# Kernel optimization log

Hardware: AMD Instinct MI355X
Metric: run time of the kernel (lower is better)

The kernel has to match this reference:

```python
import jax, jax.numpy as jnp
import numpy as np

N_NODES = 20000
N_EDGES = 320000
F_IN = 256
HID = 256
N_CLS = 5


def _glorot(key, shape):
    lim = np.sqrt(6.0 / (shape[0] + shape[1]))
    return jax.random.uniform(key, shape, jnp.float32, -lim, lim)


def setup_inputs() -> dict:
    key = jax.random.key(0)
    ks = jax.random.split(key, 12)
    x1 = jax.random.normal(ks[0], (N_NODES, F_IN), jnp.float32)
    x2 = jax.random.normal(ks[1], (N_NODES, F_IN), jnp.float32)
    ei1 = jax.random.randint(ks[2], (2, N_EDGES), 0, N_NODES, jnp.int64 if jax.config.jax_enable_x64 else jnp.int32)
    ei2 = jax.random.randint(ks[3], (2, N_EDGES), 0, N_NODES, jnp.int64 if jax.config.jax_enable_x64 else jnp.int32)
    params = {
        'W1': _glorot(ks[4], (F_IN, HID)), 'b1': jnp.zeros((HID,), jnp.float32),
        'W2': _glorot(ks[5], (HID, HID)), 'b2': jnp.zeros((HID,), jnp.float32),
        'W3': _glorot(ks[6], (HID, HID)), 'b3': jnp.zeros((HID,), jnp.float32),
        'Wl': _glorot(ks[7], (HID, N_CLS)), 'bl': jnp.zeros((N_CLS,), jnp.float32),
    }
    return {'x1': x1, 'edge_index1': ei1, 'x2': x2, 'edge_index2': ei2, **params}


def gcn_conv(x, edge_index, W, b):
    # PyG GCNConv: add self-loops, symmetric normalization D^-1/2 (A+I) D^-1/2 (X W) + b
    N = x.shape[0]
    src, dst = edge_index[0], edge_index[1]
    deg = jax.ops.segment_sum(jnp.ones(src.shape[0], x.dtype), dst, num_segments=N) + 1.0
    dinv = jax.lax.rsqrt(deg)  # [N]
    xw = x @ W                 # [N, H]
    coef = (dinv[src] * dinv[dst])[:, None]  # per-edge norm
    agg = jax.ops.segment_sum(xw[src] * coef, dst, num_segments=N)
    agg = agg + xw * (dinv * dinv)[:, None]  # self-loop term
    return agg + b


def _branch(x, ei, W1, b1, W2, b2, W3, b3):
    # dropout is identity in eval mode
    h = jax.nn.relu(gcn_conv(x, ei, W1, b1))
    h = jax.nn.relu(gcn_conv(h, ei, W2, b2))
    return gcn_conv(h, ei, W3, b3)


def reference(x1, edge_index1, x2, edge_index2, W1, b1, W2, b2, W3, b3, Wl, bl):
    h1 = _branch(x1, edge_index1, W1, b1, W2, b2, W3, b3)
    h2 = _branch(x2, edge_index2, W1, b1, W2, b2, W3, b3)
    h = jnp.concatenate([h1, h2], axis=0)          # [2N, H]
    pooled = jnp.mean(h, axis=0, keepdims=True)    # batch is all zeros -> single mean pool
    return pooled @ Wl + bl                        # [1, num_classes]
```

## Files before the change

### kernel.cpp

```cpp
#include <hip/hip_runtime.h>
#include <hip/hip_bf16.h>

#define N_NODES 20000
#define N_EDGES 320000
#define HID 256

typedef __attribute__((ext_vector_type(8))) short bf16x8;
typedef __attribute__((ext_vector_type(4))) float f32x4;

__device__ __forceinline__ float bf2f(ushort u) {
  union { unsigned int i; float f; } v; v.i = ((unsigned int)u) << 16; return v.f;
}
__device__ __forceinline__ ushort f2bf(float f) {
  union { float f; unsigned int i; } v; v.f = f;
  unsigned int r = v.i + 0x7FFFu + ((v.i >> 16) & 1u);
  return (ushort)(r >> 16);
}

__global__ void detect_kernel(const void* x1, const void* ei1, int* flags) {
  __shared__ int cnt_wild, cnt_oddnz;
  if (threadIdx.x == 0) { cnt_wild = 0; cnt_oddnz = 0; }
  __syncthreads();
  const ushort* xu = (const ushort*)x1;
  int wild = 0;
#pragma unroll
  for (int k = 0; k < 4; k++) {
    ushort u = xu[threadIdx.x * 4 + k];
    int ex = (u >> 7) & 0xFF;
    if (ex >= 0x90) wild++;
  }
  if (wild) atomicAdd(&cnt_wild, wild);
  const int* ii = (const int*)ei1;
  if (ii[threadIdx.x * 2 + 1] != 0) atomicAdd(&cnt_oddnz, 1);
  __syncthreads();
  if (threadIdx.x == 0) {
    flags[0] = (cnt_wild > 64) ? 1 : 0;
    flags[1] = (cnt_oddnz < 8) ? 1 : 0;
  }
}

__global__ void init_kernel(int* cnt0, int* cnt1, float* t0, float* t1,
                            float* s0, float* s1) {
  int i = blockIdx.x * blockDim.x + threadIdx.x;
  if (i < N_NODES) { cnt0[i] = 0; cnt1[i] = 0; t0[i] = 0.f; t1[i] = 0.f; }
  if (i < HID) { s0[i] = 0.f; s1[i] = 0.f; }
}

__global__ void cvt_ei_count_kernel(const void* e0, const void* e1,
                                    int* o0, int* o1,
                                    int* cnt0, int* cnt1,
                                    int* rank0, int* rank1, const int* flags) {
  int b = blockIdx.y;
  const void* e = b ? e1 : e0;
  int* o = b ? o1 : o0;
  int* cnt = b ? cnt1 : cnt0;
  int* rank = b ? rank1 : rank0;
  int i = blockIdx.x * 256 + threadIdx.x;
  if (i >= 2 * N_EDGES) return;
  int v = flags[1] ? (int)((const long long*)e)[i] : ((const int*)e)[i];
  o[i] = v;
  if (i >= N_EDGES) rank[i - N_EDGES] = atomicAdd(&cnt[v], 1);
}

__global__ void cvt_x_kernel(const void* x0, const void* x1v,
                             ushort* o0, ushort* o1, const int* flags) {
  const void* x = blockIdx.y ? x1v : x0;
  ushort* o = blockIdx.y ? o1 : o0;
  int i4 = (blockIdx.x * 256 + threadIdx.x) * 4;
  if (i4 >= N_NODES * HID) return;
  if (flags[0]) {
    float4 v = *(const float4*)((const float*)x + i4);
    ushort4 w; w.x = f2bf(v.x); w.y = f2bf(v.y); w.z = f2bf(v.z); w.w = f2bf(v.w);
    *(ushort4*)(o + i4) = w;
  } else {
    *(ushort4*)(o + i4) = *(const ushort4*)((const ushort*)x + i4);
  }
}

__global__ void cvt_w_kernel(const void* W1, const void* W2, const void* W3, const void* Wl,
                             const void* b1, const void* b2, const void* b3, const void* bl,
                             ushort* out, const int* flags) {
  int i = blockIdx.x * 256 + threadIdx.x;
  if (i >= 198661) return;
  const void* src; int off;
  if (i < 65536)       { src = W1; off = 0; }
  else if (i < 131072) { src = W2; off = 65536; }
  else if (i < 196608) { src = W3; off = 131072; }
  else if (i < 197888) { src = Wl; off = 196608; }
  else if (i < 198144) { src = b1; off = 197888; }
  else if (i < 198400) { src = b2; off = 198144; }
  else if (i < 198656) { src = b3; off = 198400; }
  else                 { src = bl; off = 198656; }
  int j = i - off;
  out[i] = flags[0] ? f2bf(((const float*)src)[j]) : ((const ushort*)src)[j];
}

__global__ void dinv_kernel(const int* cnt0, const int* cnt1, float* dinv0, float* dinv1) {
  int i = blockIdx.x * blockDim.x + threadIdx.x;
  if (i >= N_NODES) return;
  const int* cnt = blockIdx.y ? cnt1 : cnt0;
  float* dinv = blockIdx.y ? dinv1 : dinv0;
  dinv[i] = rsqrtf((float)cnt[i] + 1.0f);
}

__global__ __launch_bounds__(1024) void scan_kernel(const int* cnt0, const int* cnt1,
                                                    int* rp0, int* rp1) {
  const int* cnt = blockIdx.x ? cnt1 : cnt0;
  int* rp = blockIdx.x ? rp1 : rp0;
  __shared__ int sd[1024];
  int tid = threadIdx.x;
  int base = tid * 20;
  int pref[20];
  int run = 0;
#pragma unroll
  for (int k = 0; k < 20; k++) {
    int i = base + k;
    run += (i < N_NODES) ? cnt[i] : 0;
    pref[k] = run;
  }
  sd[tid] = run;
  __syncthreads();
  for (int off = 1; off < 1024; off <<= 1) {
    int v = (tid >= off) ? sd[tid - off] : 0;
    __syncthreads();
    sd[tid] += v;
    __syncthreads();
  }
  int offset = sd[tid] - run;
  if (tid == 0) rp[0] = 0;
#pragma unroll
  for (int k = 0; k < 20; k++) {
    int i = base + k;
    if (i < N_NODES) rp[i + 1] = offset + pref[k];
  }
}

__global__ void fill_kernel(const int* ei0, const int* ei1,
                            const float* dinv0, const float* dinv1,
                            const int* rp0, const int* rp1,
                            const int* rank0, const int* rank1,
                            int* col0, int* col1,
                            float* coef0, float* coef1,
                            float* t0, float* t1) {
  int e = blockIdx.x * blockDim.x + threadIdx.x;
  if (e >= N_EDGES) return;
  int b = blockIdx.y;
  const int* ei = b ? ei1 : ei0;
  const float* dinv = b ? dinv1 : dinv0;
  const int* rp = b ? rp1 : rp0;
  const int* rank = b ? rank1 : rank0;
  int* col = b ? col1 : col0;
  float* coef = b ? coef1 : coef0;
  float* t = b ? t1 : t0;
  int src = ei[e], dst = ei[N_EDGES + e];
  int slot = rp[dst] + rank[e];
  float dd = dinv[dst];
  col[slot] = src;
  coef[slot] = dinv[src] * dd;
  atomicAdd(&t[src], dd);
}

__global__ __launch_bounds__(256) void gemm_kernel(
    const ushort* __restrict__ A0, const ushort* __restrict__ A1,
    const ushort* __restrict__ W,
    ushort* __restrict__ C0, ushort* __restrict__ C1) {
  const ushort* A = blockIdx.z ? A1 : A0;
  ushort* C = blockIdx.z ? C1 : C0;
  int m0 = blockIdx.x * 64;
  int n0 = blockIdx.y * 64;
  __shared__ ushort As[64][40];
  __shared__ ushort Bs[64][40];
  int tid = threadIdx.x;
  int wave = tid >> 6, lane = tid & 63;
  int quad = lane >> 4, r16 = lane & 15;
  f32x4 acc0 = {0.f, 0.f, 0.f, 0.f}, acc1 = acc0, acc2 = acc0, acc3 = acc0;
  int la_row = tid >> 2;
  int la_off = (tid & 3) * 8;
  int lb_k = tid >> 3;
  int lb_n = (tid & 7) * 8;
  for (int k0 = 0; k0 < 256; k0 += 32) {
    int gr = m0 + la_row;
    int4 va = {0, 0, 0, 0};
    if (gr < N_NODES) va = *(const int4*)(A + gr * 256 + k0 + la_off);
    *(int4*)&As[la_row][la_off] = va;
    int4 vb = *(const int4*)(W + (k0 + lb_k) * 256 + n0 + lb_n);
    ushort tmp[8];
    *(int4*)tmp = vb;
#pragma unroll
    for (int j = 0; j < 8; j++) Bs[lb_n + j][lb_k] = tmp[j];
    __syncthreads();
    bf16x8 a  = *(const bf16x8*)&As[wave * 16 + r16][quad * 8];
    bf16x8 b0 = *(const bf16x8*)&Bs[r16][quad * 8];
    bf16x8 b1 = *(const bf16x8*)&Bs[16 + r16][quad * 8];
    bf16x8 b2 = *(const bf16x8*)&Bs[32 + r16][quad * 8];
    bf16x8 b3 = *(const bf16x8*)&Bs[48 + r16][quad * 8];
    acc0 = __builtin_amdgcn_mfma_f32_16x16x32_bf16(a, b0, acc0, 0, 0, 0);
    acc1 = __builtin_amdgcn_mfma_f32_16x16x32_bf16(a, b1, acc1, 0, 0, 0);
    acc2 = __builtin_amdgcn_mfma_f32_16x16x32_bf16(a, b2, acc2, 0, 0, 0);
    acc3 = __builtin_amdgcn_mfma_f32_16x16x32_bf16(a, b3, acc3, 0, 0, 0);
    __syncthreads();
  }
  int orow = m0 + wave * 16 + quad * 4;
#pragma unroll
  for (int r = 0; r < 4; r++) {
    int gr = orow + r;
    if (gr < N_NODES) {
      ushort* cp = C + gr * 256 + n0 + r16;
      cp[0]  = f2bf(acc0[r]);
      cp[16] = f2bf(acc1[r]);
      cp[32] = f2bf(acc2[r]);
      cp[48] = f2bf(acc3[r]);
    }
  }
}

__global__ __launch_bounds__(256) void agg_kernel(
    const ushort* __restrict__ XW0, const ushort* __restrict__ XW1,
    const float* __restrict__ dinv0, const float* __restrict__ dinv1,
    const int* __restrict__ rp0, const int* __restrict__ rp1,
    const int* __restrict__ col0, const int* __restrict__ col1,
    const float* __restrict__ coef0, const float* __restrict__ coef1,
    const ushort* __restrict__ bias,
    ushort* __restrict__ H0, ushort* __restrict__ H1) {
  int b = blockIdx.y;
  const ushort* XW = b ? XW1 : XW0;
  const float* dinv = b ? dinv1 : dinv0;
  const int* rp = b ? rp1 : rp0;
  const int* col = b ? col1 : col0;
  const float* coef = b ? coef1 : coef0;
  ushort* H = b ? H1 : H0;
  int wave = threadIdx.x >> 6, lane = threadIdx.x & 63;
  int i = blockIdx.x * 4 + wave;
  int f4 = lane * 4;
  float di = dinv[i];
  float self = di * di;
  ushort4 v = *(const ushort4*)(XW + i * 256 + f4);
  float a0 = self * bf2f(v.x), a1 = self * bf2f(v.y);
  float a2 = self * bf2f(v.z), a3 = self * bf2f(v.w);
  float c0_ = 0.f, c1_ = 0.f, c2_ = 0.f, c3_ = 0.f;
  int e0 = rp[i], e1 = rp[i + 1];
  int e = e0;
  for (; e + 3 < e1; e += 4) {
    int s0 = col[e], s1 = col[e + 1], s2 = col[e + 2], s3 = col[e + 3];
    float w0 = coef[e], w1 = coef[e + 1], w2 = coef[e + 2], w3 = coef[e + 3];
    ushort4 u0 = *(const ushort4*)(XW + s0 * 256 + f4);
    ushort4 u1 = *(const ushort4*)(XW + s1 * 256 + f4);
    ushort4 u2 = *(const ushort4*)(XW + s2 * 256 + f4);
    ushort4 u3 = *(const ushort4*)(XW + s3 * 256 + f4);
    a0 += w0 * bf2f(u0.x); a1 += w0 * bf2f(u0.y); a2 += w0 * bf2f(u0.z); a3 += w0 * bf2f(u0.w);
    c0_ += w1 * bf2f(u1.x); c1_ += w1 * bf2f(u1.y); c2_ += w1 * bf2f(u1.z); c3_ += w1 * bf2f(u1.w);
    a0 += w2 * bf2f(u2.x); a1 += w2 * bf2f(u2.y); a2 += w2 * bf2f(u2.z); a3 += w2 * bf2f(u2.w);
    c0_ += w3 * bf2f(u3.x); c1_ += w3 * bf2f(u3.y); c2_ += w3 * bf2f(u3.z); c3_ += w3 * bf2f(u3.w);
  }
  for (; e < e1; e++) {
    int s = col[e];
    float c = coef[e];
    ushort4 u = *(const ushort4*)(XW + s * 256 + f4);
    a0 += c * bf2f(u.x); a1 += c * bf2f(u.y); a2 += c * bf2f(u.z); a3 += c * bf2f(u.w);
  }
  a0 += c0_; a1 += c1_; a2 += c2_; a3 += c3_;
  ushort4 bb = *(const ushort4*)(bias + f4);
  a0 = fmaxf(a0 + bf2f(bb.x), 0.f);
  a1 = fmaxf(a1 + bf2f(bb.y), 0.f);
  a2 = fmaxf(a2 + bf2f(bb.z), 0.f);
  a3 = fmaxf(a3 + bf2f(bb.w), 0.f);
  ushort4 o; o.x = f2bf(a0); o.y = f2bf(a1); o.z = f2bf(a2); o.w = f2bf(a3);
  *(ushort4*)(H + i * 256 + f4) = o;
}

__global__ __launch_bounds__(256) void colsum_kernel(
    const ushort* __restrict__ H0, const ushort* __restrict__ H1,
    const float* __restrict__ dinv0, const float* __restrict__ dinv1,
    const float* __restrict__ t0, const float* __restrict__ t1,
    float* __restrict__ s0, float* __restrict__ s1) {
  int b = blockIdx.y;
  const ushort* H = b ? H1 : H0;
  const float* dinv = b ? dinv1 : dinv0;
  const float* t = b ? t1 : t0;
  float* s = b ? s1 : s0;
  int f = threadIdx.x;
  float acc = 0.f;
  for (int j = blockIdx.x; j < N_NODES; j += gridDim.x) {
    float dj = dinv[j];
    float c = dj * (t[j] + dj);
    acc += c * bf2f(H[j * 256 + f]);
  }
  atomicAdd(&s[f], acc);
}

__global__ __launch_bounds__(256) void final_kernel(
    const float* __restrict__ s0, const float* __restrict__ s1,
    const ushort* __restrict__ W3, const ushort* __restrict__ b3,
    const ushort* __restrict__ Wl, const ushort* __restrict__ bl,
    void* __restrict__ out, const int* __restrict__ flags) {
  __shared__ float v[256];
  __shared__ float pooled[256];
  int t = threadIdx.x;
  v[t] = s0[t] + s1[t];
  __syncthreads();
  float acc = 0.f;
  for (int f = 0; f < 256; f++) acc += v[f] * bf2f(W3[f * 256 + t]);
  pooled[t] = acc * (1.0f / (2.0f * N_NODES)) + bf2f(b3[t]);
  __syncthreads();
  if (t < 5) {
    float o = bf2f(bl[t]);
    for (int h = 0; h < 256; h++) o += pooled[h] * bf2f(Wl[h * 5 + t]);
    if (flags[0]) ((float*)out)[t] = o;
    else ((ushort*)out)[t] = f2bf(o);
  }
}

extern "C" void kernel_launch(void* const* d_in, const int* in_sizes, int n_in,
                              void* d_out, int out_size, void* d_ws, size_t ws_size,
                              hipStream_t stream) {
  const void* x1 = d_in[0];
  const void* ei1 = d_in[1];
  const void* x2 = d_in[2];
  const void* ei2 = d_in[3];
  const void* W1 = d_in[4];
  const void* b1 = d_in[5];
  const void* W2 = d_in[6];
  const void* b2 = d_in[7];
  const void* W3 = d_in[8];
  const void* b3 = d_in[9];
  const void* Wl = d_in[10];
  const void* bl = d_in[11];

  char* p = (char*)d_ws;
  auto alloc = [&](size_t bytes) {
    char* r = p;
    p += (bytes + 255) & ~size_t(255);
    return r;
  };
  int* flags   = (int*)alloc(256);
  float* dinv0 = (float*)alloc(N_NODES * 4);
  float* dinv1 = (float*)alloc(N_NODES * 4);
  float* t0    = (float*)alloc(N_NODES * 4);
  float* t1    = (float*)alloc(N_NODES * 4);
  float* s0    = (float*)alloc(HID * 4);
  float* s1    = (float*)alloc(HID * 4);
  int* cnt0    = (int*)alloc(N_NODES * 4);
  int* cnt1    = (int*)alloc(N_NODES * 4);
  int* rp0     = (int*)alloc((N_NODES + 1) * 4);
  int* rp1     = (int*)alloc((N_NODES + 1) * 4);
  int* col0    = (int*)alloc(N_EDGES * 4);
  int* col1    = (int*)alloc(N_EDGES * 4);
  float* coef0 = (float*)alloc(N_EDGES * 4);
  float* coef1 = (float*)alloc(N_EDGES * 4);
  ushort* wbuf = (ushort*)alloc(198661 * 2);
  ushort* xw0  = (ushort*)alloc((size_t)N_NODES * HID * 2);
  ushort* xw1  = (ushort*)alloc((size_t)N_NODES * HID * 2);
  ushort* xc0  = (ushort*)alloc((size_t)N_NODES * HID * 2);
  ushort* xc1  = (ushort*)alloc((size_t)N_NODES * HID * 2);
  int* ei32_0 = (int*)xw0;
  int* ei32_1 = ei32_0 + 2 * N_EDGES;
  int* rank0  = ei32_1 + 2 * N_EDGES;
  int* rank1  = rank0 + N_EDGES;
  ushort* h0 = xc0;
  ushort* h1 = xc1;

  ushort* Wc1 = wbuf + 0;
  ushort* Wc2 = wbuf + 65536;
  ushort* Wc3 = wbuf + 131072;
  ushort* Wlc = wbuf + 196608;
  ushort* bc1 = wbuf + 197888;
  ushort* bc2 = wbuf + 198144;
  ushort* bc3 = wbuf + 198400;
  ushort* blc = wbuf + 198656;

  detect_kernel<<<1, 256, 0, stream>>>(x1, ei1, flags);
  init_kernel<<<(N_NODES + 255) / 256, 256, 0, stream>>>(cnt0, cnt1, t0, t1, s0, s1);
  cvt_ei_count_kernel<<<dim3((2 * N_EDGES + 255) / 256, 2), 256, 0, stream>>>(
      ei1, ei2, ei32_0, ei32_1, cnt0, cnt1, rank0, rank1, flags);
  cvt_x_kernel<<<dim3(N_NODES * HID / 1024, 2), 256, 0, stream>>>(
      x1, x2, xc0, xc1, flags);
  cvt_w_kernel<<<(198661 + 255) / 256, 256, 0, stream>>>(
      W1, W2, W3, Wl, b1, b2, b3, bl, wbuf, flags);
  dinv_kernel<<<dim3((N_NODES + 255) / 256, 2), 256, 0, stream>>>(cnt0, cnt1, dinv0, dinv1);
  scan_kernel<<<2, 1024, 0, stream>>>(cnt0, cnt1, rp0, rp1);
  fill_kernel<<<dim3((N_EDGES + 255) / 256, 2), 256, 0, stream>>>(
      ei32_0, ei32_1, dinv0, dinv1, rp0, rp1, rank0, rank1, col0, col1, coef0, coef1, t0, t1);

  gemm_kernel<<<dim3(313, 4, 2), 256, 0, stream>>>(xc0, xc1, Wc1, xw0, xw1);
  agg_kernel<<<dim3(N_NODES / 4, 2), 256, 0, stream>>>(
      xw0, xw1, dinv0, dinv1, rp0, rp1, col0, col1, coef0, coef1, bc1, h0, h1);

  gemm_kernel<<<dim3(313, 4, 2), 256, 0, stream>>>(h0, h1, Wc2, xw0, xw1);
  agg_kernel<<<dim3(N_NODES / 4, 2), 256, 0, stream>>>(
      xw0, xw1, dinv0, dinv1, rp0, rp1, col0, col1, coef0, coef1, bc2, h0, h1);

  colsum_kernel<<<dim3(128, 2), 256, 0, stream>>>(h0, h1, dinv0, dinv1, t0, t1, s0, s1);
  final_kernel<<<1, 256, 0, stream>>>(s0, s1, Wc3, bc3, Wlc, blc, d_out, flags);
}
```

Measured before the change: 416.5 us.

## Build CSR with node-partitioned shared-memory histograms and packed edge pairs

Replaces the global-atomic edge counting and fill with node-range-partitioned kernels: 64 blocks per graph each scan all edges and use shared-memory atomics for counts, ranks and the t accumulation. This removes the init and int64-to-int32 conversion kernels and the rank buffer. Column index and coefficient are packed into one int2 array, so aggregation needs one load per edge. The column sum writes per-block partials that the final kernel reduces, replacing global float atomics. In exchange every block rereads the full edge list, and slot order within a row is nondeterministic.

```diff
diff --git a/kernel.cpp b/kernel.cpp
--- a/kernel.cpp
+++ b/kernel.cpp
@@ -4,6 +4,7 @@
 #define N_NODES 20000
 #define N_EDGES 320000
 #define HID 256
+#define NR 313
 
 typedef __attribute__((ext_vector_type(8))) short bf16x8;
 typedef __attribute__((ext_vector_type(4))) float f32x4;
@@ -37,29 +38,6 @@
     flags[0] = (cnt_wild > 64) ? 1 : 0;
     flags[1] = (cnt_oddnz < 8) ? 1 : 0;
   }
-}
-
-__global__ void init_kernel(int* cnt0, int* cnt1, float* t0, float* t1,
-                            float* s0, float* s1) {
-  int i = blockIdx.x * blockDim.x + threadIdx.x;
-  if (i < N_NODES) { cnt0[i] = 0; cnt1[i] = 0; t0[i] = 0.f; t1[i] = 0.f; }
-  if (i < HID) { s0[i] = 0.f; s1[i] = 0.f; }
-}
-
-__global__ void cvt_ei_count_kernel(const void* e0, const void* e1,
-                                    int* o0, int* o1,
-                                    int* cnt0, int* cnt1,
-                                    int* rank0, int* rank1, const int* flags) {
-  int b = blockIdx.y;
-  const void* e = b ? e1 : e0;
-  int* o = b ? o1 : o0;
-  int* cnt = b ? cnt1 : cnt0;
-  int* rank = b ? rank1 : rank0;
-  int i = blockIdx.x * 256 + threadIdx.x;
-  if (i >= 2 * N_EDGES) return;
-  int v = flags[1] ? (int)((const long long*)e)[i] : ((const int*)e)[i];
-  o[i] = v;
-  if (i >= N_EDGES) rank[i - N_EDGES] = atomicAdd(&cnt[v], 1);
 }
 
 __global__ void cvt_x_kernel(const void* x0, const void* x1v,
@@ -95,6 +73,42 @@
   out[i] = flags[0] ? f2bf(((const float*)src)[j]) : ((const ushort*)src)[j];
 }
 
+__global__ __launch_bounds__(1024) void count_part_kernel(
+    const void* e0, const void* e1, int* cnt0, int* cnt1, const int* flags) {
+  int b = blockIdx.y;
+  const void* e = b ? e1 : e0;
+  int* cnt = b ? cnt1 : cnt0;
+  int lo = blockIdx.x * NR;
+  int hi = min(lo + NR, N_NODES);
+  int nr = hi - lo;
+  __shared__ int h[NR];
+  for (int k = threadIdx.x; k < nr; k += 1024) h[k] = 0;
+  __syncthreads();
+  if (flags[1]) {
+    const long long* d = (const long long*)e + N_EDGES;
+    for (int i = threadIdx.x * 4; i < N_EDGES; i += 4096) {
+      longlong2 p0 = *(const longlong2*)(d + i);
+      longlong2 p1 = *(const longlong2*)(d + i + 2);
+      int v0 = (int)p0.x, v1 = (int)p0.y, v2 = (int)p1.x, v3 = (int)p1.y;
+      if ((unsigned)(v0 - lo) < (unsigned)nr) atomicAdd(&h[v0 - lo], 1);
+      if ((unsigned)(v1 - lo) < (unsigned)nr) atomicAdd(&h[v1 - lo], 1);
+      if ((unsigned)(v2 - lo) < (unsigned)nr) atomicAdd(&h[v2 - lo], 1);
+      if ((unsigned)(v3 - lo) < (unsigned)nr) atomicAdd(&h[v3 - lo], 1);
+    }
+  } else {
+    const int* d = (const int*)e + N_EDGES;
+    for (int i = threadIdx.x * 4; i < N_EDGES; i += 4096) {
+      int4 v = *(const int4*)(d + i);
+      if ((unsigned)(v.x - lo) < (unsigned)nr) atomicAdd(&h[v.x - lo], 1);
+      if ((unsigned)(v.y - lo) < (unsigned)nr) atomicAdd(&h[v.y - lo], 1);
+      if ((unsigned)(v.z - lo) < (unsigned)nr) atomicAdd(&h[v.z - lo], 1);
+      if ((unsigned)(v.w - lo) < (unsigned)nr) atomicAdd(&h[v.w - lo], 1);
+    }
+  }
+  __syncthreads();
+  for (int k = threadIdx.x; k < nr; k += 1024) cnt[lo + k] = h[k];
+}
+
 __global__ void dinv_kernel(const int* cnt0, const int* cnt1, float* dinv0, float* dinv1) {
   int i = blockIdx.x * blockDim.x + threadIdx.x;
   if (i >= N_NODES) return;
@@ -135,29 +149,62 @@
   }
 }
 
-__global__ void fill_kernel(const int* ei0, const int* ei1,
-                            const float* dinv0, const float* dinv1,
-                            const int* rp0, const int* rp1,
-                            const int* rank0, const int* rank1,
-                            int* col0, int* col1,
-                            float* coef0, float* coef1,
-                            float* t0, float* t1) {
-  int e = blockIdx.x * blockDim.x + threadIdx.x;
-  if (e >= N_EDGES) return;
+__global__ __launch_bounds__(1024) void fill_part_kernel(
+    const void* e0, const void* e1,
+    const float* dinv0, const float* dinv1,
+    const int* rp0, const int* rp1,
+    int2* eg0, int2* eg1, float* t0, float* t1, const int* flags) {
   int b = blockIdx.y;
-  const int* ei = b ? ei1 : ei0;
+  const void* e = b ? e1 : e0;
   const float* dinv = b ? dinv1 : dinv0;
   const int* rp = b ? rp1 : rp0;
-  const int* rank = b ? rank1 : rank0;
-  int* col = b ? col1 : col0;
-  float* coef = b ? coef1 : coef0;
+  int2* eg = b ? eg1 : eg0;
   float* t = b ? t1 : t0;
-  int src = ei[e], dst = ei[N_EDGES + e];
-  int slot = rp[dst] + rank[e];
-  float dd = dinv[dst];
-  col[slot] = src;
-  coef[slot] = dinv[src] * dd;
-  atomicAdd(&t[src], dd);
+  int lo = blockIdx.x * NR;
+  int hi = min(lo + NR, N_NODES);
+  int nr = hi - lo;
+  __shared__ int lrank[NR];
+  __shared__ int lrp[NR];
+  __shared__ float ldv[NR];
+  __shared__ float lt[NR];
+  for (int k = threadIdx.x; k < nr; k += 1024) {
+    lrank[k] = 0; lt[k] = 0.f; lrp[k] = rp[lo + k]; ldv[k] = dinv[lo + k];
+  }
+  __syncthreads();
+  bool w64 = flags[1] != 0;
+  const int* si32 = (const int*)e;
+  const int* di32 = (const int*)e + N_EDGES;
+  const long long* si64 = (const long long*)e;
+  const long long* di64 = (const long long*)e + N_EDGES;
+  for (int i = threadIdx.x * 4; i < N_EDGES; i += 4096) {
+    int s[4], d[4];
+    if (w64) {
+      longlong2 a0 = *(const longlong2*)(si64 + i);
+      longlong2 a1 = *(const longlong2*)(si64 + i + 2);
+      longlong2 b0 = *(const longlong2*)(di64 + i);
+      longlong2 b1 = *(const longlong2*)(di64 + i + 2);
+      s[0] = (int)a0.x; s[1] = (int)a0.y; s[2] = (int)a1.x; s[3] = (int)a1.y;
+      d[0] = (int)b0.x; d[1] = (int)b0.y; d[2] = (int)b1.x; d[3] = (int)b1.y;
+    } else {
+      int4 a = *(const int4*)(si32 + i);
+      int4 bb = *(const int4*)(di32 + i);
+      s[0] = a.x; s[1] = a.y; s[2] = a.z; s[3] = a.w;
+      d[0] = bb.x; d[1] = bb.y; d[2] = bb.z; d[3] = bb.w;
+    }
+#pragma unroll
+    for (int k = 0; k < 4; k++) {
+      unsigned dd = (unsigned)(d[k] - lo);
+      if (dd < (unsigned)nr) {
+        int r = atomicAdd(&lrank[dd], 1);
+        float cf = dinv[s[k]] * ldv[dd];
+        eg[lrp[dd] + r] = make_int2(s[k], __float_as_int(cf));
+      }
+      unsigned ss = (unsigned)(s[k] - lo);
+      if (ss < (unsigned)nr) atomicAdd(&lt[ss], dinv[d[k]]);
+    }
+  }
+  __syncthreads();
+  for (int k = threadIdx.x; k < nr; k += 1024) t[lo + k] = lt[k];
 }
 
 __global__ __launch_bounds__(256) void gemm_kernel(
@@ -218,16 +265,14 @@
     const ushort* __restrict__ XW0, const ushort* __restrict__ XW1,
     const float* __restrict__ dinv0, const float* __restrict__ dinv1,
     const int* __restrict__ rp0, const int* __restrict__ rp1,
-    const int* __restrict__ col0, const int* __restrict__ col1,
-    const float* __restrict__ coef0, const float* __restrict__ coef1,
+    const int2* __restrict__ eg0, const int2* __restrict__ eg1,
     const ushort* __restrict__ bias,
     ushort* __restrict__ H0, ushort* __restrict__ H1) {
   int b = blockIdx.y;
   const ushort* XW = b ? XW1 : XW0;
   const float* dinv = b ? dinv1 : dinv0;
   const int* rp = b ? rp1 : rp0;
-  const int* col = b ? col1 : col0;
-  const float* coef = b ? coef1 : coef0;
+  const int2* eg = b ? eg1 : eg0;
   ushort* H = b ? H1 : H0;
   int wave = threadIdx.x >> 6, lane = threadIdx.x & 63;
   int i = blockIdx.x * 4 + wave;
@@ -241,21 +286,22 @@
   int e0 = rp[i], e1 = rp[i + 1];
   int e = e0;
   for (; e + 3 < e1; e += 4) {
-    int s0 = col[e], s1 = col[e + 1], s2 = col[e + 2], s3 = col[e + 3];
-    float w0 = coef[e], w1 = coef[e + 1], w2 = coef[e + 2], w3 = coef[e + 3];
-    ushort4 u0 = *(const ushort4*)(XW + s0 * 256 + f4);
-    ushort4 u1 = *(const ushort4*)(XW + s1 * 256 + f4);
-    ushort4 u2 = *(const ushort4*)(XW + s2 * 256 + f4);
-    ushort4 u3 = *(const ushort4*)(XW + s3 * 256 + f4);
+    int2 p0 = eg[e], p1 = eg[e + 1], p2 = eg[e + 2], p3 = eg[e + 3];
+    ushort4 u0 = *(const ushort4*)(XW + p0.x * 256 + f4);
+    ushort4 u1 = *(const ushort4*)(XW + p1.x * 256 + f4);
+    ushort4 u2 = *(const ushort4*)(XW + p2.x * 256 + f4);
+    ushort4 u3 = *(const ushort4*)(XW + p3.x * 256 + f4);
+    float w0 = __int_as_float(p0.y), w1 = __int_as_float(p1.y);
+    float w2 = __int_as_float(p2.y), w3 = __int_as_float(p3.y);
     a0 += w0 * bf2f(u0.x); a1 += w0 * bf2f(u0.y); a2 += w0 * bf2f(u0.z); a3 += w0 * bf2f(u0.w);
     c0_ += w1 * bf2f(u1.x); c1_ += w1 * bf2f(u1.y); c2_ += w1 * bf2f(u1.z); c3_ += w1 * bf2f(u1.w);
     a0 += w2 * bf2f(u2.x); a1 += w2 * bf2f(u2.y); a2 += w2 * bf2f(u2.z); a3 += w2 * bf2f(u2.w);
     c0_ += w3 * bf2f(u3.x); c1_ += w3 * bf2f(u3.y); c2_ += w3 * bf2f(u3.z); c3_ += w3 * bf2f(u3.w);
   }
   for (; e < e1; e++) {
-    int s = col[e];
-    float c = coef[e];
-    ushort4 u = *(const ushort4*)(XW + s * 256 + f4);
+    int2 pp = eg[e];
+    float c = __int_as_float(pp.y);
+    ushort4 u = *(const ushort4*)(XW + pp.x * 256 + f4);
     a0 += c * bf2f(u.x); a1 += c * bf2f(u.y); a2 += c * bf2f(u.z); a3 += c * bf2f(u.w);
   }
   a0 += c0_; a1 += c1_; a2 += c2_; a3 += c3_;
@@ -272,31 +318,45 @@
     const ushort* __restrict__ H0, const ushort* __restrict__ H1,
     const float* __restrict__ dinv0, const float* __restrict__ dinv1,
     const float* __restrict__ t0, const float* __restrict__ t1,
-    float* __restrict__ s0, float* __restrict__ s1) {
+    float* __restrict__ P) {
   int b = blockIdx.y;
   const ushort* H = b ? H1 : H0;
   const float* dinv = b ? dinv1 : dinv0;
   const float* t = b ? t1 : t0;
-  float* s = b ? s1 : s0;
-  int f = threadIdx.x;
-  float acc = 0.f;
-  for (int j = blockIdx.x; j < N_NODES; j += gridDim.x) {
+  int wave = threadIdx.x >> 6, lane = threadIdx.x & 63;
+  int wid = blockIdx.x * 4 + wave;
+  int f4 = lane * 4;
+  float a0 = 0.f, a1 = 0.f, a2 = 0.f, a3 = 0.f;
+  for (int j = wid; j < N_NODES; j += 256) {
     float dj = dinv[j];
     float c = dj * (t[j] + dj);
-    acc += c * bf2f(H[j * 256 + f]);
-  }
-  atomicAdd(&s[f], acc);
+    ushort4 u = *(const ushort4*)(H + j * 256 + f4);
+    a0 += c * bf2f(u.x); a1 += c * bf2f(u.y);
+    a2 += c * bf2f(u.z); a3 += c * bf2f(u.w);
+  }
+  __shared__ float part[4][256];
+  part[wave][f4 + 0] = a0; part[wave][f4 + 1] = a1;
+  part[wave][f4 + 2] = a2; part[wave][f4 + 3] = a3;
+  __syncthreads();
+  int f = threadIdx.x;
+  float ssum = part[0][f] + part[1][f] + part[2][f] + part[3][f];
+  P[(b * 64 + blockIdx.x) * 256 + f] = ssum;
 }
 
 __global__ __launch_bounds__(256) void final_kernel(
-    const float* __restrict__ s0, const float* __restrict__ s1,
+    const float* __restrict__ P,
     const ushort* __restrict__ W3, const ushort* __restrict__ b3,
     const ushort* __restrict__ Wl, const ushort* __restrict__ bl,
     void* __restrict__ out, const int* __restrict__ flags) {
   __shared__ float v[256];
   __shared__ float pooled[256];
   int t = threadIdx.x;
-  v[t] = s0[t] + s1[t];
+  float acc0 = 0.f, acc1 = 0.f;
+  for (int b = 0; b < 64; b++) {
+    acc0 += P[b * 256 + t];
+    acc1 += P[(64 + b) * 256 + t];
+  }
+  v[t] = acc0 + acc1;
   __syncthreads();
   float acc = 0.f;
   for (int f = 0; f < 256; f++) acc += v[f] * bf2f(W3[f * 256 + t]);
@@ -337,25 +397,18 @@
   float* dinv1 = (float*)alloc(N_NODES * 4);
   float* t0    = (float*)alloc(N_NODES * 4);
   float* t1    = (float*)alloc(N_NODES * 4);
-  float* s0    = (float*)alloc(HID * 4);
-  float* s1    = (float*)alloc(HID * 4);
   int* cnt0    = (int*)alloc(N_NODES * 4);
   int* cnt1    = (int*)alloc(N_NODES * 4);
   int* rp0     = (int*)alloc((N_NODES + 1) * 4);
   int* rp1     = (int*)alloc((N_NODES + 1) * 4);
-  int* col0    = (int*)alloc(N_EDGES * 4);
-  int* col1    = (int*)alloc(N_EDGES * 4);
-  float* coef0 = (float*)alloc(N_EDGES * 4);
-  float* coef1 = (float*)alloc(N_EDGES * 4);
+  int2* eg0    = (int2*)alloc((size_t)N_EDGES * 8);
+  int2* eg1    = (int2*)alloc((size_t)N_EDGES * 8);
+  float* Pp    = (float*)alloc(2 * 64 * 256 * 4);
   ushort* wbuf = (ushort*)alloc(198661 * 2);
   ushort* xw0  = (ushort*)alloc((size_t)N_NODES * HID * 2);
   ushort* xw1  = (ushort*)alloc((size_t)N_NODES * HID * 2);
   ushort* xc0  = (ushort*)alloc((size_t)N_NODES * HID * 2);
   ushort* xc1  = (ushort*)alloc((size_t)N_NODES * HID * 2);
-  int* ei32_0 = (int*)xw0;
-  int* ei32_1 = ei32_0 + 2 * N_EDGES;
-  int* rank0  = ei32_1 + 2 * N_EDGES;
-  int* rank1  = rank0 + N_EDGES;
   ushort* h0 = xc0;
   ushort* h1 = xc1;
 
@@ -369,26 +422,24 @@
   ushort* blc = wbuf + 198656;
 
   detect_kernel<<<1, 256, 0, stream>>>(x1, ei1, flags);
-  init_kernel<<<(N_NODES + 255) / 256, 256, 0, stream>>>(cnt0, cnt1, t0, t1, s0, s1);
-  cvt_ei_count_kernel<<<dim3((2 * N_EDGES + 255) / 256, 2), 256, 0, stream>>>(
-      ei1, ei2, ei32_0, ei32_1, cnt0, cnt1, rank0, rank1, flags);
   cvt_x_kernel<<<dim3(N_NODES * HID / 1024, 2), 256, 0, stream>>>(
       x1, x2, xc0, xc1, flags);
   cvt_w_kernel<<<(198661 + 255) / 256, 256, 0, stream>>>(
       W1, W2, W3, Wl, b1, b2, b3, bl, wbuf, flags);
+  count_part_kernel<<<dim3(64, 2), 1024, 0, stream>>>(ei1, ei2, cnt0, cnt1, flags);
   dinv_kernel<<<dim3((N_NODES + 255) / 256, 2), 256, 0, stream>>>(cnt0, cnt1, dinv0, dinv1);
   scan_kernel<<<2, 1024, 0, stream>>>(cnt0, cnt1, rp0, rp1);
-  fill_kernel<<<dim3((N_EDGES + 255) / 256, 2), 256, 0, stream>>>(
-      ei32_0, ei32_1, dinv0, dinv1, rp0, rp1, rank0, rank1, col0, col1, coef0, coef1, t0, t1);
+  fill_part_kernel<<<dim3(64, 2), 1024, 0, stream>>>(
+      ei1, ei2, dinv0, dinv1, rp0, rp1, eg0, eg1, t0, t1, flags);
 
   gemm_kernel<<<dim3(313, 4, 2), 256, 0, stream>>>(xc0, xc1, Wc1, xw0, xw1);
   agg_kernel<<<dim3(N_NODES / 4, 2), 256, 0, stream>>>(
-      xw0, xw1, dinv0, dinv1, rp0, rp1, col0, col1, coef0, coef1, bc1, h0, h1);
+      xw0, xw1, dinv0, dinv1, rp0, rp1, eg0, eg1, bc1, h0, h1);
 
   gemm_kernel<<<dim3(313, 4, 2), 256, 0, stream>>>(h0, h1, Wc2, xw0, xw1);
   agg_kernel<<<dim3(N_NODES / 4, 2), 256, 0, stream>>>(
-      xw0, xw1, dinv0, dinv1, rp0, rp1, col0, col1, coef0, coef1, bc2, h0, h1);
-
-  colsum_kernel<<<dim3(128, 2), 256, 0, stream>>>(h0, h1, dinv0, dinv1, t0, t1, s0, s1);
-  final_kernel<<<1, 256, 0, stream>>>(s0, s1, Wc3, bc3, Wlc, blc, d_out, flags);
-}
+      xw0, xw1, dinv0, dinv1, rp0, rp1, eg0, eg1, bc2, h0, h1);
+
+  colsum_kernel<<<dim3(64, 2), 256, 0, stream>>>(h0, h1, dinv0, dinv1, t0, t1, Pp);
+  final_kernel<<<1, 256, 0, stream>>>(Pp, Wc3, bc3, Wlc, blc, d_out, flags);
+}
```

Measured after the change: 480.0 us. +15.3%, slower.

## Interleave CSR col/coef, fold dinv into scan, deterministic colsum partials

Applied to the files above, without the earlier changes.

Packs the column index and edge coefficient into a single int2 array, so the aggregation kernel issues one 8-byte load per edge instead of two separate 4-byte loads. The dinv computation moves into the scan kernel, which removes one launch. The colsum kernel now uses per-wave vectorized ushort4 reads and writes per-block partials that final_kernel reduces, replacing the atomics and the zeroing of the s buffers. Costs are a slightly larger edge array footprint and a serial 64-step reduction in the final kernel.

```diff
diff --git a/kernel.cpp b/kernel.cpp
--- a/kernel.cpp
+++ b/kernel.cpp
@@ -39,11 +39,9 @@
   }
 }
 
-__global__ void init_kernel(int* cnt0, int* cnt1, float* t0, float* t1,
-                            float* s0, float* s1) {
+__global__ void init_kernel(int* cnt0, int* cnt1, float* t0, float* t1) {
   int i = blockIdx.x * blockDim.x + threadIdx.x;
   if (i < N_NODES) { cnt0[i] = 0; cnt1[i] = 0; t0[i] = 0.f; t1[i] = 0.f; }
-  if (i < HID) { s0[i] = 0.f; s1[i] = 0.f; }
 }
 
 __global__ void cvt_ei_count_kernel(const void* e0, const void* e1,
@@ -95,18 +93,12 @@
   out[i] = flags[0] ? f2bf(((const float*)src)[j]) : ((const ushort*)src)[j];
 }
 
-__global__ void dinv_kernel(const int* cnt0, const int* cnt1, float* dinv0, float* dinv1) {
-  int i = blockIdx.x * blockDim.x + threadIdx.x;
-  if (i >= N_NODES) return;
-  const int* cnt = blockIdx.y ? cnt1 : cnt0;
-  float* dinv = blockIdx.y ? dinv1 : dinv0;
-  dinv[i] = rsqrtf((float)cnt[i] + 1.0f);
-}
-
 __global__ __launch_bounds__(1024) void scan_kernel(const int* cnt0, const int* cnt1,
-                                                    int* rp0, int* rp1) {
+                                                    int* rp0, int* rp1,
+                                                    float* dinv0, float* dinv1) {
   const int* cnt = blockIdx.x ? cnt1 : cnt0;
   int* rp = blockIdx.x ? rp1 : rp0;
+  float* dinv = blockIdx.x ? dinv1 : dinv0;
   __shared__ int sd[1024];
   int tid = threadIdx.x;
   int base = tid * 20;
@@ -115,7 +107,9 @@
 #pragma unroll
   for (int k = 0; k < 20; k++) {
     int i = base + k;
-    run += (i < N_NODES) ? cnt[i] : 0;
+    int c = (i < N_NODES) ? cnt[i] : 0;
+    if (i < N_NODES) dinv[i] = rsqrtf((float)c + 1.0f);
+    run += c;
     pref[k] = run;
   }
   sd[tid] = run;
@@ -139,8 +133,7 @@
                             const float* dinv0, const float* dinv1,
                             const int* rp0, const int* rp1,
                             const int* rank0, const int* rank1,
-                            int* col0, int* col1,
-                            float* coef0, float* coef1,
+                            int2* eg0, int2* eg1,
                             float* t0, float* t1) {
   int e = blockIdx.x * blockDim.x + threadIdx.x;
   if (e >= N_EDGES) return;
@@ -149,14 +142,12 @@
   const float* dinv = b ? dinv1 : dinv0;
   const int* rp = b ? rp1 : rp0;
   const int* rank = b ? rank1 : rank0;
-  int* col = b ? col1 : col0;
-  float* coef = b ? coef1 : coef0;
+  int2* eg = b ? eg1 : eg0;
   float* t = b ? t1 : t0;
   int src = ei[e], dst = ei[N_EDGES + e];
   int slot = rp[dst] + rank[e];
   float dd = dinv[dst];
-  col[slot] = src;
-  coef[slot] = dinv[src] * dd;
+  eg[slot] = make_int2(src, __float_as_int(dinv[src] * dd));
   atomicAdd(&t[src], dd);
 }
 
@@ -218,16 +209,14 @@
     const ushort* __restrict__ XW0, const ushort* __restrict__ XW1,
     const float* __restrict__ dinv0, const float* __restrict__ dinv1,
     const int* __restrict__ rp0, const int* __restrict__ rp1,
-    const int* __restrict__ col0, const int* __restrict__ col1,
-    const float* __restrict__ coef0, const float* __restrict__ coef1,
+    const int2* __restrict__ eg0, const int2* __restrict__ eg1,
     const ushort* __restrict__ bias,
     ushort* __restrict__ H0, ushort* __restrict__ H1) {
   int b = blockIdx.y;
   const ushort* XW = b ? XW1 : XW0;
   const float* dinv = b ? dinv1 : dinv0;
   const int* rp = b ? rp1 : rp0;
-  const int* col = b ? col1 : col0;
-  const float* coef = b ? coef1 : coef0;
+  const int2* eg = b ? eg1 : eg0;
   ushort* H = b ? H1 : H0;
   int wave = threadIdx.x >> 6, lane = threadIdx.x & 63;
   int i = blockIdx.x * 4 + wave;
@@ -241,21 +230,22 @@
   int e0 = rp[i], e1 = rp[i + 1];
   int e = e0;
   for (; e + 3 < e1; e += 4) {
-    int s0 = col[e], s1 = col[e + 1], s2 = col[e + 2], s3 = col[e + 3];
-    float w0 = coef[e], w1 = coef[e + 1], w2 = coef[e + 2], w3 = coef[e + 3];
-    ushort4 u0 = *(const ushort4*)(XW + s0 * 256 + f4);
-    ushort4 u1 = *(const ushort4*)(XW + s1 * 256 + f4);
-    ushort4 u2 = *(const ushort4*)(XW + s2 * 256 + f4);
-    ushort4 u3 = *(const ushort4*)(XW + s3 * 256 + f4);
+    int2 p0 = eg[e], p1 = eg[e + 1], p2 = eg[e + 2], p3 = eg[e + 3];
+    ushort4 u0 = *(const ushort4*)(XW + p0.x * 256 + f4);
+    ushort4 u1 = *(const ushort4*)(XW + p1.x * 256 + f4);
+    ushort4 u2 = *(const ushort4*)(XW + p2.x * 256 + f4);
+    ushort4 u3 = *(const ushort4*)(XW + p3.x * 256 + f4);
+    float w0 = __int_as_float(p0.y), w1 = __int_as_float(p1.y);
+    float w2 = __int_as_float(p2.y), w3 = __int_as_float(p3.y);
     a0 += w0 * bf2f(u0.x); a1 += w0 * bf2f(u0.y); a2 += w0 * bf2f(u0.z); a3 += w0 * bf2f(u0.w);
     c0_ += w1 * bf2f(u1.x); c1_ += w1 * bf2f(u1.y); c2_ += w1 * bf2f(u1.z); c3_ += w1 * bf2f(u1.w);
     a0 += w2 * bf2f(u2.x); a1 += w2 * bf2f(u2.y); a2 += w2 * bf2f(u2.z); a3 += w2 * bf2f(u2.w);
     c0_ += w3 * bf2f(u3.x); c1_ += w3 * bf2f(u3.y); c2_ += w3 * bf2f(u3.z); c3_ += w3 * bf2f(u3.w);
   }
   for (; e < e1; e++) {
-    int s = col[e];
-    float c = coef[e];
-    ushort4 u = *(const ushort4*)(XW + s * 256 + f4);
+    int2 pp = eg[e];
+    float c = __int_as_float(pp.y);
+    ushort4 u = *(const ushort4*)(XW + pp.x * 256 + f4);
     a0 += c * bf2f(u.x); a1 += c * bf2f(u.y); a2 += c * bf2f(u.z); a3 += c * bf2f(u.w);
   }
   a0 += c0_; a1 += c1_; a2 += c2_; a3 += c3_;
@@ -272,31 +262,45 @@
     const ushort* __restrict__ H0, const ushort* __restrict__ H1,
     const float* __restrict__ dinv0, const float* __restrict__ dinv1,
     const float* __restrict__ t0, const float* __restrict__ t1,
-    float* __restrict__ s0, float* __restrict__ s1) {
+    float* __restrict__ P) {
   int b = blockIdx.y;
   const ushort* H = b ? H1 : H0;
   const float* dinv = b ? dinv1 : dinv0;
   const float* t = b ? t1 : t0;
-  float* s = b ? s1 : s0;
-  int f = threadIdx.x;
-  float acc = 0.f;
-  for (int j = blockIdx.x; j < N_NODES; j += gridDim.x) {
+  int wave = threadIdx.x >> 6, lane = threadIdx.x & 63;
+  int wid = blockIdx.x * 4 + wave;
+  int f4 = lane * 4;
+  float a0 = 0.f, a1 = 0.f, a2 = 0.f, a3 = 0.f;
+  for (int j = wid; j < N_NODES; j += 256) {
     float dj = dinv[j];
     float c = dj * (t[j] + dj);
-    acc += c * bf2f(H[j * 256 + f]);
-  }
-  atomicAdd(&s[f], acc);
+    ushort4 u = *(const ushort4*)(H + j * 256 + f4);
+    a0 += c * bf2f(u.x); a1 += c * bf2f(u.y);
+    a2 += c * bf2f(u.z); a3 += c * bf2f(u.w);
+  }
+  __shared__ float part[4][256];
+  part[wave][f4 + 0] = a0; part[wave][f4 + 1] = a1;
+  part[wave][f4 + 2] = a2; part[wave][f4 + 3] = a3;
+  __syncthreads();
+  int f = threadIdx.x;
+  float ssum = part[0][f] + part[1][f] + part[2][f] + part[3][f];
+  P[(b * 64 + blockIdx.x) * 256 + f] = ssum;
 }
 
 __global__ __launch_bounds__(256) void final_kernel(
-    const float* __restrict__ s0, const float* __restrict__ s1,
+    const float* __restrict__ P,
     const ushort* __restrict__ W3, const ushort* __restrict__ b3,
     const ushort* __restrict__ Wl, const ushort* __restrict__ bl,
     void* __restrict__ out, const int* __restrict__ flags) {
   __shared__ float v[256];
   __shared__ float pooled[256];
   int t = threadIdx.x;
-  v[t] = s0[t] + s1[t];
+  float acc0 = 0.f, acc1 = 0.f;
+  for (int b = 0; b < 64; b++) {
+    acc0 += P[b * 256 + t];
+    acc1 += P[(64 + b) * 256 + t];
+  }
+  v[t] = acc0 + acc1;
   __syncthreads();
   float acc = 0.f;
   for (int f = 0; f < 256; f++) acc += v[f] * bf2f(W3[f * 256 + t]);
@@ -337,16 +341,13 @@
   float* dinv1 = (float*)alloc(N_NODES * 4);
   float* t0    = (float*)alloc(N_NODES * 4);
   float* t1    = (float*)alloc(N_NODES * 4);
-  float* s0    = (float*)alloc(HID * 4);
-  float* s1    = (float*)alloc(HID * 4);
   int* cnt0    = (int*)alloc(N_NODES * 4);
   int* cnt1    = (int*)alloc(N_NODES * 4);
   int* rp0     = (int*)alloc((N_NODES + 1) * 4);
   int* rp1     = (int*)alloc((N_NODES + 1) * 4);
-  int* col0    = (int*)alloc(N_EDGES * 4);
-  int* col1    = (int*)alloc(N_EDGES * 4);
-  float* coef0 = (float*)alloc(N_EDGES * 4);
-  float* coef1 = (float*)alloc(N_EDGES * 4);
+  int2* eg0    = (int2*)alloc((size_t)N_EDGES * 8);
+  int2* eg1    = (int2*)alloc((size_t)N_EDGES * 8);
+  float* Pp    = (float*)alloc(2 * 64 * 256 * 4);
   ushort* wbuf = (ushort*)alloc(198661 * 2);
   ushort* xw0  = (ushort*)alloc((size_t)N_NODES * HID * 2);
   ushort* xw1  = (ushort*)alloc((size_t)N_NODES * HID * 2);
@@ -369,26 +370,25 @@
   ushort* blc = wbuf + 198656;
 
   detect_kernel<<<1, 256, 0, stream>>>(x1, ei1, flags);
-  init_kernel<<<(N_NODES + 255) / 256, 256, 0, stream>>>(cnt0, cnt1, t0, t1, s0, s1);
+  init_kernel<<<(N_NODES + 255) / 256, 256, 0, stream>>>(cnt0, cnt1, t0, t1);
   cvt_ei_count_kernel<<<dim3((2 * N_EDGES + 255) / 256, 2), 256, 0, stream>>>(
       ei1, ei2, ei32_0, ei32_1, cnt0, cnt1, rank0, rank1, flags);
   cvt_x_kernel<<<dim3(N_NODES * HID / 1024, 2), 256, 0, stream>>>(
       x1, x2, xc0, xc1, flags);
   cvt_w_kernel<<<(198661 + 255) / 256, 256, 0, stream>>>(
       W1, W2, W3, Wl, b1, b2, b3, bl, wbuf, flags);
-  dinv_kernel<<<dim3((N_NODES + 255) / 256, 2), 256, 0, stream>>>(cnt0, cnt1, dinv0, dinv1);
-  scan_kernel<<<2, 1024, 0, stream>>>(cnt0, cnt1, rp0, rp1);
+  scan_kernel<<<2, 1024, 0, stream>>>(cnt0, cnt1, rp0, rp1, dinv0, dinv1);
   fill_kernel<<<dim3((N_EDGES + 255) / 256, 2), 256, 0, stream>>>(
-      ei32_0, ei32_1, dinv0, dinv1, rp0, rp1, rank0, rank1, col0, col1, coef0, coef1, t0, t1);
+      ei32_0, ei32_1, dinv0, dinv1, rp0, rp1, rank0, rank1, eg0, eg1, t0, t1);
 
   gemm_kernel<<<dim3(313, 4, 2), 256, 0, stream>>>(xc0, xc1, Wc1, xw0, xw1);
   agg_kernel<<<dim3(N_NODES / 4, 2), 256, 0, stream>>>(
-      xw0, xw1, dinv0, dinv1, rp0, rp1, col0, col1, coef0, coef1, bc1, h0, h1);
+      xw0, xw1, dinv0, dinv1, rp0, rp1, eg0, eg1, bc1, h0, h1);
 
   gemm_kernel<<<dim3(313, 4, 2), 256, 0, stream>>>(h0, h1, Wc2, xw0, xw1);
   agg_kernel<<<dim3(N_NODES / 4, 2), 256, 0, stream>>>(
-      xw0, xw1, dinv0, dinv1, rp0, rp1, col0, col1, coef0, coef1, bc2, h0, h1);
-
-  colsum_kernel<<<dim3(128, 2), 256, 0, stream>>>(h0, h1, dinv0, dinv1, t0, t1, s0, s1);
-  final_kernel<<<1, 256, 0, stream>>>(s0, s1, Wc3, bc3, Wlc, blc, d_out, flags);
-}
+      xw0, xw1, dinv0, dinv1, rp0, rp1, eg0, eg1, bc2, h0, h1);
+
+  colsum_kernel<<<dim3(64, 2), 256, 0, stream>>>(h0, h1, dinv0, dinv1, t0, t1, Pp);
+  final_kernel<<<1, 256, 0, stream>>>(Pp, Wc3, bc3, Wlc, blc, d_out, flags);
+}
```

After: 414.5 us. No clear change (-0.5%).
